# Kernel tuning notes

Hardware: AMD Instinct MI355X
Metric: run time of the kernel (lower is better)

The kernel has to match this reference:

```python
import jax, jax.numpy as jnp
import numpy as np

N, L, H, DH = 4, 1024, 16, 64
D = H * DH  # 1024
DFF = 4 * D
NEG_INF = jnp.float32(-1e30)  # used via actual -inf per torch masked_fill


def layer_norm(x, g, b, eps=1e-5):
    mu = jnp.mean(x, axis=-1, keepdims=True)
    var = jnp.mean(jnp.square(x - mu), axis=-1, keepdims=True)
    return (x - mu) * jax.lax.rsqrt(var + eps) * g + b


def mha(q_in, k_in, Wq, Wk, Wv, mask, padding_mask):
    # q_in: (N,Lq,D), k_in: (N,Lk,D); Linear weights (D,D), out = x @ W.T
    n, Lq, _ = q_in.shape
    Lk = k_in.shape[1]
    q = jnp.einsum('nld,od->nlo', q_in, Wq).reshape(n, Lq, H, DH)
    k = jnp.einsum('nld,od->nlo', k_in, Wk).reshape(n, Lk, H, DH)
    v = jnp.einsum('nld,od->nlo', k_in, Wv).reshape(n, Lk, H, DH)
    # per-sample scaling = sqrt(#non-padded keys)
    scaling = jnp.sqrt(jnp.sum(~padding_mask, axis=-1).astype(q.dtype))  # (N,)
    score = jnp.einsum('nqhd,nkhd->nhqk', q, k) / scaling[:, None, None, None]
    if mask is not None:
        score = jnp.where(mask[None, None, :, :], -jnp.inf, score)
    score = jnp.where(padding_mask[:, None, None, :], -jnp.inf, score)
    p = jax.nn.softmax(score, axis=-1)
    out = jnp.einsum('nhqk,nkhd->nqhd', p, v).reshape(n, Lq, D)
    return out


def setup_inputs() -> dict:
    key = jax.random.key(0)
    ks = jax.random.split(key, 16)
    s = 0.02
    inp = {
        'encoded': jax.random.normal(ks[0], (N, L, D), jnp.float32),
        'Y': jax.random.normal(ks[1], (N, L, D), jnp.float32),
        # causal mask: True above diagonal -> attention set to -inf
        'mask': ~jnp.tril(jnp.ones((L, L), dtype=bool)),
        # suffix padding with varied per-sample lengths (all >= 1)
        'padding_mask': jnp.arange(L)[None, :] >= jnp.array([L, 3 * L // 4, L // 2, 7 * L // 8])[:, None],
        # masked self-attention projections
        'Wq1': jax.random.normal(ks[2], (D, D), jnp.float32) * s,
        'Wk1': jax.random.normal(ks[3], (D, D), jnp.float32) * s,
        'Wv1': jax.random.normal(ks[4], (D, D), jnp.float32) * s,
        'g1': jnp.ones((D,), jnp.float32), 'b1': jnp.zeros((D,), jnp.float32),
        # cross-attention projections
        'Wq2': jax.random.normal(ks[5], (D, D), jnp.float32) * s,
        'Wk2': jax.random.normal(ks[6], (D, D), jnp.float32) * s,
        'Wv2': jax.random.normal(ks[7], (D, D), jnp.float32) * s,
        'g2': jnp.ones((D,), jnp.float32), 'b2': jnp.zeros((D,), jnp.float32),
        # FFN
        'We': jax.random.normal(ks[8], (DFF, D), jnp.float32) * s,
        'be': jnp.zeros((DFF,), jnp.float32),
        'Wc': jax.random.normal(ks[9], (D, DFF), jnp.float32) * s,
        'bc': jnp.zeros((D,), jnp.float32),
        'g3': jnp.ones((D,), jnp.float32), 'b3': jnp.zeros((D,), jnp.float32),
    }
    return inp


def reference(encoded, Y, mask, padding_mask,
              Wq1, Wk1, Wv1, g1, b1,
              Wq2, Wk2, Wv2, g2, b2,
              We, be, Wc, bc, g3, b3):
    # masked self-attention + residual + LN (dropout=0 -> identity)
    res = Y
    a = mha(Y, Y, Wq1, Wk1, Wv1, mask, padding_mask)
    Y = layer_norm(a + res, g1, b1)
    # cross-attention (no causal mask) + residual + LN
    res = Y
    a = mha(Y, encoded, Wq2, Wk2, Wv2, None, padding_mask)
    Y = layer_norm(a + res, g2, b2)
    # FFN + residual + LN
    res = Y
    h = jax.nn.relu(jnp.einsum('nld,fd->nlf', Y, We) + be)
    h = jnp.einsum('nlf,df->nld', h, Wc) + bc
    Y = layer_norm(h + res, g3, b3)
    return Y
```

## Files before the change

### kernel.cpp

```cpp
#include <hip/hip_runtime.h>
#include <stdint.h>

#define NB 4
#define LS 1024
#define HH 16
#define DHD 64
#define DM 1024
#define DF 4096
#define QKS 2048

typedef unsigned short u16;
typedef __attribute__((ext_vector_type(4))) float f32x4;
typedef __attribute__((ext_vector_type(8))) __bf16 bf16x8;
typedef __attribute__((ext_vector_type(8))) unsigned short u16x8;

__device__ __forceinline__ u16 f2bf(float f) {
  union { float f; uint32_t u; } v; v.f = f;
  uint32_t u = v.u;
  return (u16)((u + 0x7fffu + ((u >> 16) & 1u)) >> 16);
}

__device__ __forceinline__ bf16x8 ldb8(const u16* p) {
  u16x8 r = *(const u16x8*)p;
  return __builtin_bit_cast(bf16x8, r);
}

__device__ __forceinline__ void gload_lds16(const u16* g, u16* l) {
  __builtin_amdgcn_global_load_lds((const __attribute__((address_space(1))) void*)g,
                                   (__attribute__((address_space(3))) void*)l,
                                   16, 0, 0);
}

#define WAITV8() asm volatile("s_waitcnt vmcnt(8)" ::: "memory")
#define WAITV0() asm volatile("s_waitcnt vmcnt(0)" ::: "memory")
#define WAITLGKM() asm volatile("s_waitcnt lgkmcnt(0)" ::: "memory")
#define PHASE_BARRIER()                        \
  do {                                         \
    WAITLGKM();                                \
    __builtin_amdgcn_sched_barrier(0);         \
    __builtin_amdgcn_s_barrier();              \
    __builtin_amdgcn_sched_barrier(0);         \
  } while (0)

__global__ void prep_kernel(const uint32_t* __restrict__ pm, int* lens, float* iscl) {
  __shared__ int flagByte;
  __shared__ int red[256];
  int tid = threadIdx.x;
  if (tid == 0) flagByte = 0;
  __syncthreads();
  int f = 0;
  for (int w = tid; w < (NB * LS) / 4; w += 256) {
    uint32_t u = pm[w];
    if (u != 0u && u != 1u && u != 0x3f800000u) f = 1;
  }
  if (f) atomicOr(&flagByte, 1);
  __syncthreads();
  int isByte = flagByte;
  for (int n = 0; n < NB; n++) {
    int c = 0;
    if (isByte) {
      const uint8_t* pb = (const uint8_t*)pm;
      for (int l = tid; l < LS; l += 256) c += (pb[n * LS + l] == 0) ? 1 : 0;
    } else {
      for (int l = tid; l < LS; l += 256) c += (pm[n * LS + l] == 0) ? 1 : 0;
    }
    red[tid] = c;
    __syncthreads();
    for (int s = 128; s > 0; s >>= 1) {
      if (tid < s) red[tid] += red[tid + s];
      __syncthreads();
    }
    if (tid == 0) { lens[n] = red[0]; iscl[n] = 1.0f / sqrtf((float)red[0]); }
    __syncthreads();
  }
}

__global__ void cvt_all(const float* s0, u16* d0, const float* s1, u16* d1,
                        const float* s2, u16* d2, const float* s3, u16* d3,
                        const float* s4, u16* d4, const float* s5, u16* d5,
                        const float* s6, u16* d6, const float* s7, u16* d7,
                        const float* s8, u16* d8, const float* s9, u16* d9) {
  const int total = 5767168;
  int i = blockIdx.x * 256 + threadIdx.x;
  for (; i < total; i += gridDim.x * 256) {
    const float* s; u16* d; int j;
    if (i < 1048576)      { s = s0; d = d0; j = i; }
    else if (i < 2097152) { s = s1; d = d1; j = i - 1048576; }
    else if (i < 2359296) { s = s2; d = d2; j = i - 2097152; }
    else if (i < 2621440) { s = s3; d = d3; j = i - 2359296; }
    else if (i < 2883584) { s = s4; d = d4; j = i - 2621440; }
    else if (i < 3145728) { s = s5; d = d5; j = i - 2883584; }
    else if (i < 3407872) { s = s6; d = d6; j = i - 3145728; }
    else if (i < 3670016) { s = s7; d = d7; j = i - 3407872; }
    else if (i < 4718592) { s = s8; d = d8; j = i - 3670016; }
    else                  { s = s9; d = d9; j = i - 4718592; }
    float4 fv = ((const float4*)s)[j];
    ushort4 o;
    o.x = f2bf(fv.x); o.y = f2bf(fv.y); o.z = f2bf(fv.z); o.w = f2bf(fv.w);
    ((ushort4*)d)[j] = o;
  }
}

template <int MODE>
__global__ __launch_bounds__(512, 2) void gemm8(
    const u16* __restrict__ P0, const u16* __restrict__ P1,
    const u16* __restrict__ PW, const float* __restrict__ bias,
    void* __restrict__ O0, void* __restrict__ O1,
    void* __restrict__ O2, void* __restrict__ O3) {
  extern __shared__ u16 lds[];
  constexpr int NT = 16;
  const int bm = blockIdx.x;
  const int tid = threadIdx.x;
  const int wid = tid >> 6, lane = tid & 63;
  const int lrow = lane & 15, lgrp = lane >> 4;
  const int wm = wid >> 2, wn = wid & 3;

  const u16* Asrc; const u16* Bsrc; int lda, ldb;
  if constexpr (MODE == 0) {
    Asrc = P0 + (size_t)bm * 256 * DM; lda = DM;
    Bsrc = PW + (size_t)blockIdx.y * 256 * DM; ldb = DM;
  } else if constexpr (MODE == 1) {
    const int z = blockIdx.z;
    Asrc = P0 + (size_t)bm * 256 * DF + z * 1024; lda = DF;
    Bsrc = PW + (size_t)blockIdx.y * 256 * DF + z * 1024; ldb = DF;
  } else {
    const int bnt = blockIdx.y;
    Asrc = (bnt < 12 ? P0 : P1) + (size_t)bm * 256 * DM; lda = DM;
    const int wrow = (bnt < 12) ? bnt * 256 : 4096 + (bnt - 12) * 256;
    Bsrc = PW + (size_t)wrow * DM; ldb = DM;
  }

  int srow[2], skk[2];
#pragma unroll
  for (int i = 0; i < 2; i++) {
    const int c = (i * 8 + wid) * 64 + lane;
    const int pair = c >> 3;
    const int ue = ((c & 7) * 8) ^ ((pair & 7) << 3);
    srow[i] = pair * 2 + (ue >> 5);
    skk[i] = ue & 31;
  }
  const int dslot0 = wid * 512;
  const int dslot1 = (8 + wid) * 512;

  f32x4 acc[2][4][4] = {};

  auto STAGE_A = [&](int kt, int buf, int kh) {
    const int ks = kt < NT ? kt : NT - 1;
    gload_lds16(Asrc + (size_t)srow[0] * lda + ks * 64 + kh * 32 + skk[0],
                lds + buf * 16384 + kh * 8192 + dslot0);
    gload_lds16(Asrc + (size_t)srow[1] * lda + ks * 64 + kh * 32 + skk[1],
                lds + buf * 16384 + kh * 8192 + dslot1);
  };
  auto STAGE_B = [&](int kt, int buf, int kh) {
    const int ks = kt < NT ? kt : NT - 1;
    gload_lds16(Bsrc + (size_t)srow[0] * ldb + ks * 64 + kh * 32 + skk[0],
                lds + 32768 + buf * 16384 + kh * 8192 + dslot0);
    gload_lds16(Bsrc + (size_t)srow[1] * ldb + ks * 64 + kh * 32 + skk[1],
                lds + 32768 + buf * 16384 + kh * 8192 + dslot1);
  };
  auto LDA = [&](int buf, int kh, int mh, bf16x8* a) {
#pragma unroll
    for (int m = 0; m < 4; m++) {
      const int row = wm * 128 + mh * 64 + m * 16 + lrow;
      const int idx = buf * 16384 + kh * 8192 + (row >> 1) * 64 +
                      ((((row & 1) << 5) + (lgrp << 3)) ^ (((row >> 1) & 7) << 3));
      a[m] = ldb8(lds + idx);
    }
  };
  auto LDB = [&](int buf, int kh, bf16x8* b) {
#pragma unroll
    for (int nn = 0; nn < 4; nn++) {
      const int row = wn * 64 + nn * 16 + lrow;
      const int idx = 32768 + buf * 16384 + kh * 8192 + (row >> 1) * 64 +
                      ((((row & 1) << 5) + (lgrp << 3)) ^ (((row >> 1) & 7) << 3));
      b[nn] = ldb8(lds + idx);
    }
  };
  auto MFMA16 = [&](f32x4 (&a4)[4][4], bf16x8* af, bf16x8* bk) {
    __builtin_amdgcn_s_setprio(1);
#pragma unroll
    for (int m = 0; m < 4; m++)
#pragma unroll
      for (int nn = 0; nn < 4; nn++)
        a4[m][nn] = __builtin_amdgcn_mfma_f32_16x16x32_bf16(af[m], bk[nn], a4[m][nn], 0, 0, 0);
    __builtin_amdgcn_s_setprio(0);
  };

  STAGE_A(0, 0, 0); STAGE_B(0, 0, 0);
  STAGE_A(0, 0, 1); STAGE_B(0, 0, 1);
  STAGE_A(1, 1, 0); STAGE_B(1, 1, 0);
  WAITV8();
  __builtin_amdgcn_s_barrier();
  __builtin_amdgcn_sched_barrier(0);

  for (int t = 0; t < NT; t++) {
    const int b = t & 1;
    bf16x8 af[4], bk[4];
    LDA(b, 0, 0, af); LDB(b, 0, bk);
    STAGE_A(t + 1, b ^ 1, 1);
    PHASE_BARRIER();
    MFMA16(acc[0], af, bk);
    LDA(b, 0, 1, af);
    STAGE_B(t + 1, b ^ 1, 1);
    WAITV8();
    PHASE_BARRIER();
    MFMA16(acc[1], af, bk);
    LDA(b, 1, 0, af); LDB(b, 1, bk);
    STAGE_A(t + 2, b, 0);
    PHASE_BARRIER();
    MFMA16(acc[0], af, bk);
    LDA(b, 1, 1, af);
    STAGE_B(t + 2, b, 0);
    WAITV8();
    PHASE_BARRIER();
    MFMA16(acc[1], af, bk);
  }
  WAITV0();

#pragma unroll
  for (int mh = 0; mh < 2; mh++)
#pragma unroll
    for (int m = 0; m < 4; m++) {
      const int grow0 = bm * 256 + wm * 128 + mh * 64 + m * 16 + lgrp * 4;
#pragma unroll
      for (int nn = 0; nn < 4; nn++) {
        const int col_l = wn * 64 + nn * 16 + lrow;
        f32x4 v = acc[mh][m][nn];
        if constexpr (MODE == 0) {
          const int col = blockIdx.y * 256 + col_l;
          const float bv = bias[col];
#pragma unroll
          for (int r = 0; r < 4; r++) {
            float x = v[r] + bv;
            x = x > 0.0f ? x : 0.0f;
            ((u16*)O0)[(size_t)(grow0 + r) * DF + col] = f2bf(x);
          }
        } else if constexpr (MODE == 1) {
          float* C = (float*)O0 + (size_t)blockIdx.z * ((size_t)NB * LS * DM);
          const int col = blockIdx.y * 256 + col_l;
#pragma unroll
          for (int r = 0; r < 4; r++) C[(size_t)(grow0 + r) * DM + col] = v[r];
        } else {
          const int bnt = blockIdx.y;
          const int nidx = grow0 >> 10, l0 = grow0 & 1023;
          if (bnt < 8) {
            const int col = bnt * 256 + col_l;
#pragma unroll
            for (int r = 0; r < 4; r++)
              ((u16*)O0)[(size_t)(grow0 + r) * QKS + col] = f2bf(v[r]);
          } else if (bnt < 12) {
            const int vc = (bnt - 8) * 256 + col_l;
            ushort4 o;
            o.x = f2bf(v[0]); o.y = f2bf(v[1]); o.z = f2bf(v[2]); o.w = f2bf(v[3]);
            *(ushort4*)((u16*)O1 + (((size_t)(nidx * HH + (vc >> 6)) * DHD + (vc & 63)) << 10) + l0) = o;
          } else if (bnt < 16) {
            const int col = 1024 + (bnt - 12) * 256 + col_l;
#pragma unroll
            for (int r = 0; r < 4; r++)
              ((u16*)O2)[(size_t)(grow0 + r) * QKS + col] = f2bf(v[r]);
          } else {
            const int vc = (bnt - 16) * 256 + col_l;
            ushort4 o;
            o.x = f2bf(v[0]); o.y = f2bf(v[1]); o.z = f2bf(v[2]); o.w = f2bf(v[3]);
            *(ushort4*)((u16*)O3 + (((size_t)(nidx * HH + (vc >> 6)) * DHD + (vc & 63)) << 10) + l0) = o;
          }
        }
      }
    }
}

template <int EPI>
__global__ __launch_bounds__(256) void gemm_bt(const u16* __restrict__ A, int lda,
                                               const u16* __restrict__ B, int ldb,
                                               const float* __restrict__ bias,
                                               void* __restrict__ Cout, int ldc,
                                               int Klen, size_t zcstride) {
  __shared__ u16 Al[128 * 32];
  __shared__ u16 Bl[128 * 32];
  const int tid = threadIdx.x;
  const int bm = blockIdx.x, bn = blockIdx.y, z = blockIdx.z;
  const int wave = tid >> 6, lane = tid & 63;
  const int lrow = lane & 15, lgrp = lane >> 4;
  const int wr = (wave >> 1) * 64, wc = (wave & 1) * 64;
  f32x4 acc[4][4] = {};
  const u16* Ab = A + (size_t)bm * 128 * lda + (size_t)z * Klen;
  const u16* Bb = B + (size_t)bn * 128 * ldb + (size_t)z * Klen;
  char* Cz = (char*)Cout + (size_t)z * zcstride;
  {
    const int c0 = wave, c1 = wave + 4;
    const int r0 = c0 * 16 + (lane >> 2), r1 = c1 * 16 + (lane >> 2);
    const int scc = (lane & 3) * 8;
    const u16* Ag0 = Ab + (size_t)r0 * lda + scc;
    const u16* Ag1 = Ab + (size_t)r1 * lda + scc;
    const u16* Bg0 = Bb + (size_t)r0 * ldb + scc;
    const u16* Bg1 = Bb + (size_t)r1 * ldb + scc;
    u16* Ad0 = Al + c0 * 512;
    u16* Ad1 = Al + c1 * 512;
    u16* Bd0 = Bl + c0 * 512;
    u16* Bd1 = Bl + c1 * 512;
    for (int kb = 0; kb < Klen; kb += 32) {
      gload_lds16(Ag0, Ad0);
      gload_lds16(Ag1, Ad1);
      gload_lds16(Bg0, Bd0);
      gload_lds16(Bg1, Bd1);
      Ag0 += 32; Ag1 += 32; Bg0 += 32; Bg1 += 32;
      __syncthreads();
      bf16x8 af[4], bfr[4];
#pragma unroll
      for (int m = 0; m < 4; m++) af[m] = ldb8(Al + (wr + m * 16 + lrow) * 32 + lgrp * 8);
#pragma unroll
      for (int nn = 0; nn < 4; nn++) bfr[nn] = ldb8(Bl + (wc + nn * 16 + lrow) * 32 + lgrp * 8);
#pragma unroll
      for (int m = 0; m < 4; m++)
#pragma unroll
        for (int nn = 0; nn < 4; nn++)
          acc[m][nn] = __builtin_amdgcn_mfma_f32_16x16x32_bf16(af[m], bfr[nn], acc[m][nn], 0, 0, 0);
      __syncthreads();
    }
  }
#pragma unroll
  for (int m = 0; m < 4; m++) {
    const int row0 = bm * 128 + wr + m * 16 + lgrp * 4;
#pragma unroll
    for (int nn = 0; nn < 4; nn++) {
      const int col = bn * 128 + wc + nn * 16 + lrow;
      float bv = (EPI == 1) ? bias[col] : 0.0f;
#pragma unroll
      for (int r = 0; r < 4; r++) {
        float v = acc[m][nn][r];
        if (EPI == 1) { v += bv; v = v > 0.0f ? v : 0.0f; }
        size_t idx = (size_t)(row0 + r) * ldc + col;
        if (EPI == 4) ((float*)Cz)[idx] = v;
        else ((u16*)Cz)[idx] = f2bf(v);
      }
    }
  }
}

template <bool CAUSAL>
__global__ __launch_bounds__(256) void attn_kernel(const u16* __restrict__ QK,
                                                   const u16* __restrict__ Vt,
                                                   float* __restrict__ Out,
                                                   const int* __restrict__ lens,
                                                   const float* __restrict__ iscl) {
  __shared__ u16 Kl[64 * 72];
  __shared__ u16 Vl[64 * 72];
  __shared__ u16 Pl[4][16 * 72];
  const int n = blockIdx.z, h = blockIdx.y, qb = blockIdx.x * 64;
  const int tid = threadIdx.x, wave = tid >> 6, lane = tid & 63;
  const int lrow = lane & 15, lgrp = lane >> 4;
  const int len = lens[n];
  const float isc = iscl[n];
  const int qrow = qb + wave * 16 + lrow;
  const u16* qptr = QK + ((size_t)(n * LS + qrow)) * QKS + h * DHD + lgrp * 8;
  bf16x8 qf0 = ldb8(qptr);
  bf16x8 qf1 = ldb8(qptr + 32);
  f32x4 oacc[4] = {};
  float m_run[4], l_run[4];
#pragma unroll
  for (int r = 0; r < 4; r++) { m_run[r] = -1e30f; l_run[r] = 0.0f; }
  const int kend = CAUSAL ? (len < qb + 64 ? len : qb + 64) : len;
  const int srow = tid >> 3, sc = (tid & 7) * 8;
  const u16* kg_base = QK + 1024 + ((size_t)(n * LS)) * QKS + h * DHD + sc;
  const u16* vg_base = Vt + ((size_t)((n * HH + h) * DHD) + srow) * LS + sc;
  u16* pw = Pl[wave];
  for (int kb = 0; kb < kend; kb += 64) {
    __syncthreads();
#pragma unroll
    for (int i = 0; i < 2; i++) {
      const int row = srow + i * 32;
      u16x8 kv = *(const u16x8*)(kg_base + (size_t)(kb + row) * QKS);
      *(u16x8*)(Kl + row * 72 + sc) = kv;
      u16x8 vv = *(const u16x8*)(vg_base + (size_t)(i * 32) * LS + kb);
      *(u16x8*)(Vl + row * 72 + sc) = vv;
    }
    __syncthreads();
    f32x4 s[4];
#pragma unroll
    for (int st = 0; st < 4; st++) {
      const u16* kr = Kl + (st * 16 + lrow) * 72 + lgrp * 8;
      bf16x8 kf0 = ldb8(kr);
      bf16x8 kf1 = ldb8(kr + 32);
      f32x4 z = {};
      z = __builtin_amdgcn_mfma_f32_16x16x32_bf16(qf0, kf0, z, 0, 0, 0);
      s[st] = __builtin_amdgcn_mfma_f32_16x16x32_bf16(qf1, kf1, z, 0, 0, 0);
    }
    const int q_r = qb + wave * 16 + lgrp * 4;
#pragma unroll
    for (int st = 0; st < 4; st++) {
      const int k = kb + st * 16 + lrow;
#pragma unroll
      for (int r = 0; r < 4; r++) {
        float v = s[st][r] * isc;
        bool ok = (k < len) && (!CAUSAL || k <= q_r + r);
        s[st][r] = ok ? v : -1e30f;
      }
    }
#pragma unroll
    for (int r = 0; r < 4; r++) {
      float mx = fmaxf(fmaxf(s[0][r], s[1][r]), fmaxf(s[2][r], s[3][r]));
      mx = fmaxf(mx, __shfl_xor(mx, 1));
      mx = fmaxf(mx, __shfl_xor(mx, 2));
      mx = fmaxf(mx, __shfl_xor(mx, 4));
      mx = fmaxf(mx, __shfl_xor(mx, 8));
      float mn = fmaxf(m_run[r], mx);
      float fac = __expf(m_run[r] - mn);
      m_run[r] = mn;
      float sm = 0.0f;
#pragma unroll
      for (int st = 0; st < 4; st++) {
        float p = __expf(s[st][r] - mn);
        s[st][r] = p;
        sm += p;
      }
      sm += __shfl_xor(sm, 1);
      sm += __shfl_xor(sm, 2);
      sm += __shfl_xor(sm, 4);
      sm += __shfl_xor(sm, 8);
      l_run[r] = l_run[r] * fac + sm;
#pragma unroll
      for (int dt = 0; dt < 4; dt++) oacc[dt][r] *= fac;
    }
#pragma unroll
    for (int st = 0; st < 4; st++)
#pragma unroll
      for (int r = 0; r < 4; r++)
        pw[(lgrp * 4 + r) * 72 + st * 16 + lrow] = f2bf(s[st][r]);
#pragma unroll
    for (int ks = 0; ks < 2; ks++) {
      bf16x8 pf = ldb8(pw + lrow * 72 + ks * 32 + lgrp * 8);
#pragma unroll
      for (int dt = 0; dt < 4; dt++) {
        bf16x8 vf = ldb8(Vl + (dt * 16 + lrow) * 72 + ks * 32 + lgrp * 8);
        oacc[dt] = __builtin_amdgcn_mfma_f32_16x16x32_bf16(pf, vf, oacc[dt], 0, 0, 0);
      }
    }
  }
#pragma unroll
  for (int r = 0; r < 4; r++) {
    float inv = 1.0f / l_run[r];
    const int row = qb + wave * 16 + lgrp * 4 + r;
    float* op = Out + ((size_t)(n * LS + row)) * DM + h * DHD;
#pragma unroll
    for (int dt = 0; dt < 4; dt++) op[dt * 16 + lrow] = oacc[dt][r] * inv;
  }
}

__global__ __launch_bounds__(256) void ln_kernel(const float* __restrict__ a,
                                                 const float* __restrict__ res,
                                                 const float* __restrict__ g,
                                                 const float* __restrict__ bta,
                                                 float* __restrict__ outf,
                                                 u16* __restrict__ outb) {
  const int row = blockIdx.x, tid = threadIdx.x;
  float4 x = ((const float4*)(a + (size_t)row * DM))[tid];
  float4 rr = ((const float4*)(res + (size_t)row * DM))[tid];
  x.x += rr.x; x.y += rr.y; x.z += rr.z; x.w += rr.w;
  float s = x.x + x.y + x.z + x.w;
  float s2 = x.x * x.x + x.y * x.y + x.z * x.z + x.w * x.w;
#pragma unroll
  for (int m = 1; m < 64; m <<= 1) { s += __shfl_xor(s, m); s2 += __shfl_xor(s2, m); }
  __shared__ float sm[8];
  const int wv = tid >> 6;
  if ((tid & 63) == 0) { sm[wv] = s; sm[4 + wv] = s2; }
  __syncthreads();
  s = sm[0] + sm[1] + sm[2] + sm[3];
  s2 = sm[4] + sm[5] + sm[6] + sm[7];
  const float mean = s * (1.0f / (float)DM);
  const float var = s2 * (1.0f / (float)DM) - mean * mean;
  const float inv = rsqrtf(var + 1e-5f);
  float4 gg = ((const float4*)g)[tid];
  float4 bb = ((const float4*)bta)[tid];
  float4 y;
  y.x = (x.x - mean) * inv * gg.x + bb.x;
  y.y = (x.y - mean) * inv * gg.y + bb.y;
  y.z = (x.z - mean) * inv * gg.z + bb.z;
  y.w = (x.w - mean) * inv * gg.w + bb.w;
  ((float4*)(outf + (size_t)row * DM))[tid] = y;
  if (outb) {
    ushort4 o;
    o.x = f2bf(y.x); o.y = f2bf(y.y); o.z = f2bf(y.z); o.w = f2bf(y.w);
    ((ushort4*)(outb + (size_t)row * DM))[tid] = o;
  }
}

__global__ __launch_bounds__(256) void ln_final(const float* __restrict__ part,
                                                const float* __restrict__ bias,
                                                const float* __restrict__ res,
                                                const float* __restrict__ g,
                                                const float* __restrict__ bta,
                                                float* __restrict__ outf) {
  const int row = blockIdx.x, tid = threadIdx.x;
  const size_t PS = (size_t)NB * LS * DM;
  float4 x = ((const float4*)(part + (size_t)row * DM))[tid];
  float4 p1 = ((const float4*)(part + PS + (size_t)row * DM))[tid];
  float4 p2 = ((const float4*)(part + 2 * PS + (size_t)row * DM))[tid];
  float4 p3 = ((const float4*)(part + 3 * PS + (size_t)row * DM))[tid];
  float4 bb4 = ((const float4*)bias)[tid];
  float4 rr = ((const float4*)(res + (size_t)row * DM))[tid];
  x.x += p1.x + p2.x + p3.x + bb4.x + rr.x;
  x.y += p1.y + p2.y + p3.y + bb4.y + rr.y;
  x.z += p1.z + p2.z + p3.z + bb4.z + rr.z;
  x.w += p1.w + p2.w + p3.w + bb4.w + rr.w;
  float s = x.x + x.y + x.z + x.w;
  float s2 = x.x * x.x + x.y * x.y + x.z * x.z + x.w * x.w;
#pragma unroll
  for (int m = 1; m < 64; m <<= 1) { s += __shfl_xor(s, m); s2 += __shfl_xor(s2, m); }
  __shared__ float sm[8];
  const int wv = tid >> 6;
  if ((tid & 63) == 0) { sm[wv] = s; sm[4 + wv] = s2; }
  __syncthreads();
  s = sm[0] + sm[1] + sm[2] + sm[3];
  s2 = sm[4] + sm[5] + sm[6] + sm[7];
  const float mean = s * (1.0f / (float)DM);
  const float var = s2 * (1.0f / (float)DM) - mean * mean;
  const float inv = rsqrtf(var + 1e-5f);
  float4 gg = ((const float4*)g)[tid];
  float4 bb = ((const float4*)bta)[tid];
  float4 y;
  y.x = (x.x - mean) * inv * gg.x + bb.x;
  y.y = (x.y - mean) * inv * gg.y + bb.y;
  y.z = (x.z - mean) * inv * gg.z + bb.z;
  y.w = (x.w - mean) * inv * gg.w + bb.w;
  ((float4*)(outf + (size_t)row * DM))[tid] = y;
}

extern "C" void kernel_launch(void* const* d_in, const int* in_sizes, int n_in,
                              void* d_out, int out_size, void* d_ws, size_t ws_size,
                              hipStream_t stream) {
  const float* enc = (const float*)d_in[0];
  const float* Yin = (const float*)d_in[1];
  const uint32_t* pmask = (const uint32_t*)d_in[3];
  const float* Wq1 = (const float*)d_in[4];
  const float* Wk1 = (const float*)d_in[5];
  const float* Wv1 = (const float*)d_in[6];
  const float* g1 = (const float*)d_in[7];
  const float* b1 = (const float*)d_in[8];
  const float* Wq2 = (const float*)d_in[9];
  const float* Wk2 = (const float*)d_in[10];
  const float* Wv2 = (const float*)d_in[11];
  const float* g2 = (const float*)d_in[12];
  const float* b2 = (const float*)d_in[13];
  const float* We = (const float*)d_in[14];
  const float* be = (const float*)d_in[15];
  const float* Wc = (const float*)d_in[16];
  const float* bc = (const float*)d_in[17];
  const float* g3 = (const float*)d_in[18];
  const float* b3 = (const float*)d_in[19];

  const size_t ACT = (size_t)NB * LS * DM;
  const size_t WSZ = (size_t)DM * DM;
  const size_t WFF = (size_t)DF * DM;
  const size_t HID = (size_t)NB * LS * DF;

  char* ws = (char*)d_ws;
  size_t off = 0;
  auto alloc = [&](size_t bytes) -> void* {
    void* p = ws + off;
    off += (bytes + 255) & ~(size_t)255;
    return p;
  };
  int* lens = (int*)alloc(64);
  float* iscl = (float*)alloc(64);
  u16* Ybf = (u16*)alloc(ACT * 2);
  u16* Ebf = (u16*)alloc(ACT * 2);
  u16* W6 = (u16*)alloc(WSZ * 6 * 2);
  u16* Web = (u16*)alloc(WFF * 2);
  u16* Wcb = (u16*)alloc(WFF * 2);
  size_t region0 = off;
  u16* QKa = (u16*)alloc((size_t)NB * LS * QKS * 2);
  u16* VtA = (u16*)alloc(ACT * 2);
  u16* QKb = (u16*)alloc((size_t)NB * LS * QKS * 2);
  u16* VtB = (u16*)alloc(ACT * 2);
  float* aout = (float*)alloc(ACT * 4);
  float* y2 = (float*)alloc(ACT * 4);
  float* part = (float*)(ws + region0);
  float* y3 = (float*)alloc(ACT * 4);
  u16* Hb = (u16*)alloc(HID * 2);

  prep_kernel<<<1, 256, 0, stream>>>(pmask, lens, iscl);
  cvt_all<<<2048, 256, 0, stream>>>(Yin, Ybf, enc, Ebf,
                                    Wq1, W6 + 0 * WSZ, Wk1, W6 + 1 * WSZ,
                                    Wv1, W6 + 2 * WSZ, Wq2, W6 + 3 * WSZ,
                                    Wk2, W6 + 4 * WSZ, Wv2, W6 + 5 * WSZ,
                                    We, Web, Wc, Wcb);

  dim3 blk(256);
  gemm8<2><<<dim3(16, 20), 512, 131072, stream>>>(Ybf, Ebf, W6, nullptr,
                                                  QKa, VtA, QKb, VtB);
  attn_kernel<true><<<dim3(16, 16, 4), blk, 0, stream>>>(QKa, VtA, aout, lens, iscl);
  ln_kernel<<<NB * LS, 256, 0, stream>>>(aout, Yin, g1, b1, y2, Ybf);
  gemm_bt<0><<<dim3(32, 8), blk, 0, stream>>>(Ybf, DM, W6 + 3 * WSZ, DM, nullptr,
                                              QKb, QKS, DM, 0);
  attn_kernel<false><<<dim3(16, 16, 4), blk, 0, stream>>>(QKb, VtB, aout, lens, iscl);
  ln_kernel<<<NB * LS, 256, 0, stream>>>(aout, y2, g2, b2, y3, Ebf);
  gemm8<0><<<dim3(16, 16), 512, 131072, stream>>>(Ebf, nullptr, Web, be,
                                                  Hb, nullptr, nullptr, nullptr);
  gemm8<1><<<dim3(16, 4, 4), 512, 131072, stream>>>(Hb, nullptr, Wcb, nullptr,
                                                    part, nullptr, nullptr, nullptr);
  ln_final<<<NB * LS, 256, 0, stream>>>(part, bc, y3, g3, b3, (float*)d_out);
}
```

Baseline: 347.5 us.

## Move cross-attn V projection into Q2 GEMM and parallelize mask prep per batch

The cross-attention V projection moves out of the first batched projection GEMM, which shrinks from 20 to 16 column tiles, into the later Q2 projection kernel. That kernel now covers both Q and V with a 32x16 grid, so the second GEMM launch gets twice as many blocks and the first gets fewer. The padding-length prep kernel now runs one block per batch sample instead of a single block looping over all samples. The intent is better load balance across the GPU, at the cost of the V work running in the smaller-tile 256-thread kernel.

```diff
diff --git a/kernel.cpp b/kernel.cpp
--- a/kernel.cpp
+++ b/kernel.cpp
@@ -45,7 +45,7 @@
 __global__ void prep_kernel(const uint32_t* __restrict__ pm, int* lens, float* iscl) {
   __shared__ int flagByte;
   __shared__ int red[256];
-  int tid = threadIdx.x;
+  const int tid = threadIdx.x, n = blockIdx.x;
   if (tid == 0) flagByte = 0;
   __syncthreads();
   int f = 0;
@@ -55,24 +55,20 @@
   }
   if (f) atomicOr(&flagByte, 1);
   __syncthreads();
-  int isByte = flagByte;
-  for (int n = 0; n < NB; n++) {
-    int c = 0;
-    if (isByte) {
-      const uint8_t* pb = (const uint8_t*)pm;
-      for (int l = tid; l < LS; l += 256) c += (pb[n * LS + l] == 0) ? 1 : 0;
-    } else {
-      for (int l = tid; l < LS; l += 256) c += (pm[n * LS + l] == 0) ? 1 : 0;
-    }
-    red[tid] = c;
+  int c = 0;
+  if (flagByte) {
+    const uint8_t* pb = (const uint8_t*)pm;
+    for (int l = tid; l < LS; l += 256) c += (pb[n * LS + l] == 0) ? 1 : 0;
+  } else {
+    for (int l = tid; l < LS; l += 256) c += (pm[n * LS + l] == 0) ? 1 : 0;
+  }
+  red[tid] = c;
+  __syncthreads();
+  for (int s = 128; s > 0; s >>= 1) {
+    if (tid < s) red[tid] += red[tid + s];
     __syncthreads();
-    for (int s = 128; s > 0; s >>= 1) {
-      if (tid < s) red[tid] += red[tid + s];
-      __syncthreads();
-    }
-    if (tid == 0) { lens[n] = red[0]; iscl[n] = 1.0f / sqrtf((float)red[0]); }
-    __syncthreads();
-  }
+  }
+  if (tid == 0) { lens[n] = red[0]; iscl[n] = 1.0f / sqrtf((float)red[0]); }
 }
 
 __global__ void cvt_all(const float* s0, u16* d0, const float* s1, u16* d1,
@@ -253,52 +249,48 @@
             ushort4 o;
             o.x = f2bf(v[0]); o.y = f2bf(v[1]); o.z = f2bf(v[2]); o.w = f2bf(v[3]);
             *(ushort4*)((u16*)O1 + (((size_t)(nidx * HH + (vc >> 6)) * DHD + (vc & 63)) << 10) + l0) = o;
-          } else if (bnt < 16) {
+          } else {
             const int col = 1024 + (bnt - 12) * 256 + col_l;
 #pragma unroll
             for (int r = 0; r < 4; r++)
               ((u16*)O2)[(size_t)(grow0 + r) * QKS + col] = f2bf(v[r]);
-          } else {
-            const int vc = (bnt - 16) * 256 + col_l;
-            ushort4 o;
-            o.x = f2bf(v[0]); o.y = f2bf(v[1]); o.z = f2bf(v[2]); o.w = f2bf(v[3]);
-            *(ushort4*)((u16*)O3 + (((size_t)(nidx * HH + (vc >> 6)) * DHD + (vc & 63)) << 10) + l0) = o;
           }
         }
       }
     }
 }
 
-template <int EPI>
-__global__ __launch_bounds__(256) void gemm_bt(const u16* __restrict__ A, int lda,
-                                               const u16* __restrict__ B, int ldb,
-                                               const float* __restrict__ bias,
-                                               void* __restrict__ Cout, int ldc,
-                                               int Klen, size_t zcstride) {
+__global__ __launch_bounds__(256) void gemm_qv(const u16* __restrict__ Ya,
+                                               const u16* __restrict__ Ea,
+                                               const u16* __restrict__ Wq,
+                                               const u16* __restrict__ Wv,
+                                               u16* __restrict__ QKb,
+                                               u16* __restrict__ VtB) {
   __shared__ u16 Al[128 * 32];
   __shared__ u16 Bl[128 * 32];
   const int tid = threadIdx.x;
-  const int bm = blockIdx.x, bn = blockIdx.y, z = blockIdx.z;
+  const int bm = blockIdx.x, bnr = blockIdx.y;
+  const bool isV = bnr >= 8;
+  const int bn = isV ? bnr - 8 : bnr;
   const int wave = tid >> 6, lane = tid & 63;
   const int lrow = lane & 15, lgrp = lane >> 4;
   const int wr = (wave >> 1) * 64, wc = (wave & 1) * 64;
   f32x4 acc[4][4] = {};
-  const u16* Ab = A + (size_t)bm * 128 * lda + (size_t)z * Klen;
-  const u16* Bb = B + (size_t)bn * 128 * ldb + (size_t)z * Klen;
-  char* Cz = (char*)Cout + (size_t)z * zcstride;
+  const u16* Ab = (isV ? Ea : Ya) + (size_t)bm * 128 * DM;
+  const u16* Bb = (isV ? Wv : Wq) + (size_t)bn * 128 * DM;
   {
     const int c0 = wave, c1 = wave + 4;
     const int r0 = c0 * 16 + (lane >> 2), r1 = c1 * 16 + (lane >> 2);
     const int scc = (lane & 3) * 8;
-    const u16* Ag0 = Ab + (size_t)r0 * lda + scc;
-    const u16* Ag1 = Ab + (size_t)r1 * lda + scc;
-    const u16* Bg0 = Bb + (size_t)r0 * ldb + scc;
-    const u16* Bg1 = Bb + (size_t)r1 * ldb + scc;
+    const u16* Ag0 = Ab + (size_t)r0 * DM + scc;
+    const u16* Ag1 = Ab + (size_t)r1 * DM + scc;
+    const u16* Bg0 = Bb + (size_t)r0 * DM + scc;
+    const u16* Bg1 = Bb + (size_t)r1 * DM + scc;
     u16* Ad0 = Al + c0 * 512;
     u16* Ad1 = Al + c1 * 512;
     u16* Bd0 = Bl + c0 * 512;
     u16* Bd1 = Bl + c1 * 512;
-    for (int kb = 0; kb < Klen; kb += 32) {
+    for (int kb = 0; kb < DM; kb += 32) {
       gload_lds16(Ag0, Ad0);
       gload_lds16(Ag1, Ad1);
       gload_lds16(Bg0, Bd0);
@@ -321,17 +313,20 @@
 #pragma unroll
   for (int m = 0; m < 4; m++) {
     const int row0 = bm * 128 + wr + m * 16 + lgrp * 4;
+    const int nidx = row0 >> 10, l0 = row0 & (LS - 1);
 #pragma unroll
     for (int nn = 0; nn < 4; nn++) {
       const int col = bn * 128 + wc + nn * 16 + lrow;
-      float bv = (EPI == 1) ? bias[col] : 0.0f;
-#pragma unroll
-      for (int r = 0; r < 4; r++) {
-        float v = acc[m][nn][r];
-        if (EPI == 1) { v += bv; v = v > 0.0f ? v : 0.0f; }
-        size_t idx = (size_t)(row0 + r) * ldc + col;
-        if (EPI == 4) ((float*)Cz)[idx] = v;
-        else ((u16*)Cz)[idx] = f2bf(v);
+      if (!isV) {
+#pragma unroll
+        for (int r = 0; r < 4; r++)
+          QKb[(size_t)(row0 + r) * QKS + col] = f2bf(acc[m][nn][r]);
+      } else {
+        const int hh = col >> 6, dd = col & 63;
+        ushort4 o;
+        o.x = f2bf(acc[m][nn][0]); o.y = f2bf(acc[m][nn][1]);
+        o.z = f2bf(acc[m][nn][2]); o.w = f2bf(acc[m][nn][3]);
+        *(ushort4*)(VtB + (((size_t)(nidx * HH + hh) * DHD + dd) << 10) + l0) = o;
       }
     }
   }
@@ -578,7 +573,7 @@
   float* y3 = (float*)alloc(ACT * 4);
   u16* Hb = (u16*)alloc(HID * 2);
 
-  prep_kernel<<<1, 256, 0, stream>>>(pmask, lens, iscl);
+  prep_kernel<<<NB, 256, 0, stream>>>(pmask, lens, iscl);
   cvt_all<<<2048, 256, 0, stream>>>(Yin, Ybf, enc, Ebf,
                                     Wq1, W6 + 0 * WSZ, Wk1, W6 + 1 * WSZ,
                                     Wv1, W6 + 2 * WSZ, Wq2, W6 + 3 * WSZ,
@@ -586,12 +581,12 @@
                                     We, Web, Wc, Wcb);
 
   dim3 blk(256);
-  gemm8<2><<<dim3(16, 20), 512, 131072, stream>>>(Ybf, Ebf, W6, nullptr,
+  gemm8<2><<<dim3(16, 16), 512, 131072, stream>>>(Ybf, Ebf, W6, nullptr,
                                                   QKa, VtA, QKb, VtB);
   attn_kernel<true><<<dim3(16, 16, 4), blk, 0, stream>>>(QKa, VtA, aout, lens, iscl);
   ln_kernel<<<NB * LS, 256, 0, stream>>>(aout, Yin, g1, b1, y2, Ybf);
-  gemm_bt<0><<<dim3(32, 8), blk, 0, stream>>>(Ybf, DM, W6 + 3 * WSZ, DM, nullptr,
-                                              QKb, QKS, DM, 0);
+  gemm_qv<<<dim3(32, 16), blk, 0, stream>>>(Ybf, Ebf, W6 + 3 * WSZ, W6 + 5 * WSZ,
+                                            QKb, VtB);
   attn_kernel<false><<<dim3(16, 16, 4), blk, 0, stream>>>(QKb, VtB, aout, lens, iscl);
   ln_kernel<<<NB * LS, 256, 0, stream>>>(aout, y2, g2, b2, y3, Ebf);
   gemm8<0><<<dim3(16, 16), 512, 131072, stream>>>(Ebf, nullptr, Web, be,
```

Measured after the change: 319.0 us, median of 5. 1.09x faster.
